# Kernel optimization log

Hardware: AMD Instinct MI355X
Metric: run time of the kernel (lower is better)

Reference implementation:

```python
import jax, jax.numpy as jnp
import numpy as np

N = 100000
F_IN = 128
HIDDEN = 64
HEADS = 4
EPS = 1e-16
SLOPE = 0.2  # PyG GATConv default negative_slope


def gat_conv(x, src, dst, W, a_src, a_dst, b, heads, out_ch, concat, n_nodes):
    # x: [N, F]; W: [F, heads*out_ch]; a_src/a_dst: [heads, out_ch]
    h = (x @ W).reshape(n_nodes, heads, out_ch)              # [N, H, C]
    alpha_s = jnp.einsum('nhc,hc->nh', h, a_src)             # [N, H]
    alpha_d = jnp.einsum('nhc,hc->nh', h, a_dst)             # [N, H]
    e = alpha_s[src] + alpha_d[dst]                          # [E, H]
    e = jnp.where(e > 0, e, SLOPE * e)                       # leaky_relu
    # segment softmax over destination node
    m = jax.ops.segment_max(e, dst, num_segments=n_nodes)    # [N, H]
    m = jnp.where(jnp.isfinite(m), m, 0.0)                   # empty segments
    ex = jnp.exp(e - m[dst])                                 # [E, H]
    denom = jax.ops.segment_sum(ex, dst, num_segments=n_nodes)  # [N, H]
    alpha = ex / (denom[dst] + EPS)                          # [E, H]
    # weighted scatter-aggregate of source features at destinations
    msg = h[src] * alpha[:, :, None]                         # [E, H, C]
    out = jax.ops.segment_sum(msg, dst, num_segments=n_nodes)  # [N, H, C]
    if concat:
        out = out.reshape(n_nodes, heads * out_ch)
    else:
        out = out.mean(axis=1)
    return out + b


def setup_inputs() -> dict:
    key = jax.random.key(0)
    ks = jax.random.split(key, 12)
    x = jax.random.normal(ks[0], (N, F_IN), dtype=jnp.float32)
    edge_index = jax.random.randint(ks[1], (2, 1600000), 0, N, dtype=jnp.int64)
    s1 = 1.0 / np.sqrt(F_IN)
    s2 = 1.0 / np.sqrt(HIDDEN)
    return {
        'x': x,
        'edge_index': edge_index,
        'W1': jax.random.normal(ks[2], (F_IN, HIDDEN), dtype=jnp.float32) * s1,
        'a_src1': jax.random.normal(ks[3], (HEADS, HIDDEN // HEADS), dtype=jnp.float32) * s2,
        'a_dst1': jax.random.normal(ks[4], (HEADS, HIDDEN // HEADS), dtype=jnp.float32) * s2,
        'b1': jnp.zeros((HIDDEN,), dtype=jnp.float32),
        'W2': jax.random.normal(ks[5], (HIDDEN, HIDDEN), dtype=jnp.float32) * s2,
        'a_src2': jax.random.normal(ks[6], (1, HIDDEN), dtype=jnp.float32) * s2,
        'a_dst2': jax.random.normal(ks[7], (1, HIDDEN), dtype=jnp.float32) * s2,
        'b2': jnp.zeros((HIDDEN,), dtype=jnp.float32),
        'Wc': jax.random.normal(ks[8], (HIDDEN, 1), dtype=jnp.float32) * s2,
        'bc': jnp.zeros((1,), dtype=jnp.float32),
    }


def reference(x, edge_index, W1, a_src1, a_dst1, b1, W2, a_src2, a_dst2, b2, Wc, bc):
    src, dst = edge_index[0], edge_index[1]
    # dropout layers are identity in eval mode
    h = gat_conv(x, src, dst, W1, a_src1, a_dst1, b1,
                 heads=HEADS, out_ch=HIDDEN // HEADS, concat=True, n_nodes=N)
    h = jax.nn.relu(h)
    h = gat_conv(h, src, dst, W2, a_src2, a_dst2, b2,
                 heads=1, out_ch=HIDDEN, concat=False, n_nodes=N)
    h = jax.nn.relu(h)
    return h @ Wc + bc  # [N, 1]
```

## Files before the change

kernel.cpp:

```cpp
#include <hip/hip_runtime.h>
#include <hip/hip_bf16.h>


typedef __hip_bfloat16 bf16;
typedef unsigned short ushort;
typedef unsigned char uchar;
typedef __attribute__((ext_vector_type(8))) short short8;
typedef __attribute__((ext_vector_type(4))) float f32x4;

#define NN 100000
#define EE 1600000
#define BKB 9
#define BKN (1 << BKB)
#define NBK ((NN + BKN - 1) >> BKB)
#define CAP 10240
#define TILE 4096
#define EPT 16
#define NT ((EE + TILE - 1) / TILE)
#define GH 391
#define GT 782
#define BN 16
#define CHE 512

__device__ __forceinline__ float relu_np(float v) { return (v < 0.f) ? 0.f : v; }
__device__ __forceinline__ float lrelu(float v) { return v > 0.f ? v : 0.2f * v; }
__device__ __forceinline__ ushort f2bf(float f) {
    __hip_bfloat16 h = __float2bfloat16(f);
    return *reinterpret_cast<ushort*>(&h);
}
__device__ __forceinline__ float bf2f(ushort u) {
    unsigned int x = ((unsigned int)u) << 16;
    return __uint_as_float(x);
}

__device__ __forceinline__ void gemm1_body(
    int gb, ushort* wB, ushort* wE,
    const float* __restrict__ x, const float* __restrict__ W1,
    const float* __restrict__ aS, const float* __restrict__ aD,
    ushort* __restrict__ h1, float* __restrict__ as1, float* __restrict__ ad1)
{
    const int tid = threadIdx.x;
    for (int i = tid; i < 128 * 64; i += 256) {
        int k = i >> 6, n = i & 63;
        wB[n * 128 + k] = f2bf(W1[i]);
    }
    for (int i = tid; i < 128 * 16; i += 256) {
        int k = i >> 4, j = i & 15;
        float v = 0.f;
        if (j < 8) {
            int h = j & 3;
            const float* av = (j < 4) ? aS : aD;
            for (int c = 0; c < 16; ++c)
                v = fmaf(W1[k * 64 + h * 16 + c], av[h * 16 + c], v);
        }
        wE[j * 128 + k] = f2bf(v);
    }
    __syncthreads();
    const int w = tid >> 6, lane = tid & 63;
    const int m = lane & 15, quad = lane >> 4;
    const int ntiles = NN >> 4;
    for (int tile = gb * 4 + w; tile < ntiles; tile += GT * 4) {
        const int row0 = tile << 4;
        f32x4 acc[4] = {f32x4{0,0,0,0}, f32x4{0,0,0,0},
                        f32x4{0,0,0,0}, f32x4{0,0,0,0}};
        f32x4 acc5 = {0, 0, 0, 0};
        const float* xp = x + (size_t)(row0 + m) * 128 + quad * 8;
        #pragma unroll
        for (int ks = 0; ks < 128; ks += 32) {
            f32x4 x0 = *(const f32x4*)(xp + ks);
            f32x4 x1 = *(const f32x4*)(xp + ks + 4);
            short8 a;
            #pragma unroll
            for (int j = 0; j < 4; ++j) a[j] = (short)f2bf(x0[j]);
            #pragma unroll
            for (int j = 0; j < 4; ++j) a[4 + j] = (short)f2bf(x1[j]);
            #pragma unroll
            for (int t = 0; t < 4; ++t) {
                short8 b = *(const short8*)&wB[(t * 16 + m) * 128 + ks + quad * 8];
                acc[t] = __builtin_amdgcn_mfma_f32_16x16x32_bf16(a, b, acc[t], 0, 0, 0);
            }
            short8 b5 = *(const short8*)&wE[m * 128 + ks + quad * 8];
            acc5 = __builtin_amdgcn_mfma_f32_16x16x32_bf16(a, b5, acc5, 0, 0, 0);
        }
        #pragma unroll
        for (int t = 0; t < 4; ++t)
            #pragma unroll
            for (int r = 0; r < 4; ++r)
                h1[(size_t)(row0 + quad * 4 + r) * 64 + t * 16 + m] = f2bf(acc[t][r]);
        #pragma unroll
        for (int r = 0; r < 4; ++r) {
            int row = row0 + quad * 4 + r;
            if (m < 4) as1[row * 4 + m] = acc5[r];
            else if (m < 8) ad1[row * 4 + (m - 4)] = acc5[r];
        }
    }
}

__global__ __launch_bounds__(256) void k_pg(
    const int* __restrict__ src, const int* __restrict__ dst,
    int* __restrict__ gcur, int* __restrict__ pairs,
    const float* __restrict__ x, const float* __restrict__ W1,
    const float* __restrict__ aS, const float* __restrict__ aD,
    ushort* __restrict__ h1, float* __restrict__ as1, float* __restrict__ ad1,
    const float* __restrict__ W2, const float* __restrict__ aS2,
    const float* __restrict__ aD2, ushort* __restrict__ wExt)
{
    __shared__ ushort wB[64 * 128];
    __shared__ ushort wE[16 * 128];
    __shared__ int lh[NBK];
    __shared__ int lbase[NBK];
    const int bid = blockIdx.x;
    const int tid = threadIdx.x;

    if (bid < NT) {
        for (int i = tid; i < NBK; i += 256) lh[i] = 0;
        __syncthreads();
        const int e0 = bid * TILE;
        int pk[EPT], bk[EPT], rv[EPT];
        #pragma unroll
        for (int j = 0; j < EPT; ++j) {
            int e = e0 + j * 256 + tid;
            if (e < EE) {
                int d = dst[e];
                bk[j] = d >> BKB;
                pk[j] = src[e] | ((d & (BKN - 1)) << 17);
                rv[j] = atomicAdd(&lh[bk[j]], 1);
            }
        }
        __syncthreads();
        for (int i = tid; i < NBK; i += 256)
            lbase[i] = lh[i] ? atomicAdd(&gcur[i], lh[i]) : 0;
        __syncthreads();
        #pragma unroll
        for (int j = 0; j < EPT; ++j) {
            int e = e0 + j * 256 + tid;
            if (e < EE)
                pairs[(size_t)bk[j] * CAP + lbase[bk[j]] + rv[j]] = pk[j];
        }
    } else if (bid < NT + GH) {
        gemm1_body(bid - NT, wB, wE, x, W1, aS, aD, h1, as1, ad1);
    } else {
        for (int i = tid; i < 80 * 64; i += 256) {
            int n = i >> 6, k = i & 63;
            float v = 0.f;
            if (n < 64) {
                v = W2[k * 64 + n];
            } else if (n == 64) {
                for (int c = 0; c < 64; ++c) v = fmaf(W2[k * 64 + c], aS2[c], v);
            } else if (n == 65) {
                for (int c = 0; c < 64; ++c) v = fmaf(W2[k * 64 + c], aD2[c], v);
            }
            wExt[i] = f2bf(v);
        }
    }
}

__global__ __launch_bounds__(256) void k_bg(
    const int* __restrict__ gcur, const int* __restrict__ pairs,
    int* __restrict__ row_ptr, uchar* __restrict__ rcnt,
    int* __restrict__ col,
    const float* __restrict__ x, const float* __restrict__ W1,
    const float* __restrict__ aS, const float* __restrict__ aD,
    ushort* __restrict__ h1, float* __restrict__ as1, float* __restrict__ ad1)
{
    __shared__ ushort wB[64 * 128];
    __shared__ ushort wE[16 * 128];
    __shared__ int hist[BKN];
    __shared__ int sP[256];
    const int bid = blockIdx.x;
    const int tid = threadIdx.x;

    if (bid >= NBK) {
        gemm1_body(bid - NBK + GH, wB, wE, x, W1, aS, aD, h1, as1, ad1);
        return;
    }

    const int b = bid;
    const int n0 = b << BKB;
    const int base = b * CAP, endE = base + gcur[b];
    for (int i = tid; i < BKN; i += 256) hist[i] = 0;
    __syncthreads();
    for (int i = base + tid; i < endE; i += 256)
        atomicAdd(&hist[pairs[i] >> 17], 1);
    __syncthreads();
    int a0 = hist[2 * tid], a1 = hist[2 * tid + 1];
    int tot = a0 + a1;
    sP[tid] = tot;
    __syncthreads();
    for (int off = 1; off < 256; off <<= 1) {
        int t = (tid >= off) ? sP[tid - off] : 0;
        __syncthreads();
        sP[tid] += t;
        __syncthreads();
    }
    const int excl = sP[tid] - tot;
    const int c0 = base + excl;
    hist[2 * tid] = c0;
    hist[2 * tid + 1] = c0 + a0;
    if (n0 + 2 * tid < NN) {
        row_ptr[n0 + 2 * tid] = c0;
        rcnt[n0 + 2 * tid] = (uchar)a0;
    }
    if (n0 + 2 * tid + 1 < NN) {
        row_ptr[n0 + 2 * tid + 1] = c0 + a0;
        rcnt[n0 + 2 * tid + 1] = (uchar)a1;
    }
    __syncthreads();
    for (int i = base + tid; i < endE; i += 256) {
        int pr = pairs[i];
        int p = atomicAdd(&hist[pr >> 17], 1);
        col[p] = pr & 0x1FFFF;
    }
}

__global__ __launch_bounds__(256, 8) void k_seg1f(
    const int* __restrict__ rp, const uchar* __restrict__ rcnt,
    const int* __restrict__ col,
    const float* __restrict__ as1, const float* __restrict__ ad1,
    const ushort* __restrict__ h1, const float* __restrict__ b1,
    const ushort* __restrict__ wExt,
    ushort* __restrict__ h2, float* __restrict__ as2, float* __restrict__ ad2,
    int N)
{
    __shared__ __align__(16) ushort zS[BN * 72];
    __shared__ float pS[CHE * 4];
    __shared__ int colS[CHE];
    __shared__ uchar ndS[CHE];
    __shared__ int sRp[BN + 1];
    __shared__ float bS[64];
    __shared__ float adS[BN * 4];

    const int tid = threadIdx.x;
    const int n0 = blockIdx.x * BN;

    if (tid < 64) bS[tid] = b1[tid];
    if (tid < BN * 4) adS[tid] = ad1[(size_t)n0 * 4 + tid];
    if (tid < BN) sRp[tid] = rp[n0 + tid];
    if (tid == BN) sRp[BN] = rp[n0 + BN - 1] + (int)rcnt[n0 + BN - 1];
    __syncthreads();

    const int eb0 = sRp[0];
    const int cnt = min(sRp[BN] - eb0, CHE);

    for (int t = tid; t < cnt; t += 256) {
        int ge = eb0 + t;
        colS[t] = col[ge];
        int nd = 0;
        #pragma unroll
        for (int k = 1; k < BN; ++k) nd += (ge >= sRp[k]);
        ndS[t] = (uchar)nd;
    }
    __syncthreads();
    for (int t = tid; t < cnt * 4; t += 256) {
        int e = t >> 2, hh = t & 3;
        float v = as1[(size_t)colS[e] * 4 + hh] + adS[ndS[e] * 4 + hh];
        pS[t] = __expf(lrelu(v));
    }
    __syncthreads();

    const int w = tid >> 6, lane = tid & 63;
    const int g = lane >> 4, c4 = lane & 15, head = c4 >> 2;
    const int nb = w * 4 + g;
    const int s_n = sRp[nb] - eb0, e_n = sRp[nb + 1] - eb0;

    f32x4 acc = {0, 0, 0, 0};
    float den = 0.f;
    int i = s_n;
    for (; i + 3 < e_n; i += 4) {
        int cA = colS[i], cB = colS[i + 1], cC = colS[i + 2], cD = colS[i + 3];
        ushort4 hA = *(const ushort4*)&h1[(size_t)cA * 64 + c4 * 4];
        ushort4 hB = *(const ushort4*)&h1[(size_t)cB * 64 + c4 * 4];
        ushort4 hC = *(const ushort4*)&h1[(size_t)cC * 64 + c4 * 4];
        ushort4 hD = *(const ushort4*)&h1[(size_t)cD * 64 + c4 * 4];
        float pA = pS[(i + 0) * 4 + head], pB = pS[(i + 1) * 4 + head];
        float pC = pS[(i + 2) * 4 + head], pD = pS[(i + 3) * 4 + head];
        den += (pA + pB) + (pC + pD);
        acc[0] = fmaf(pA, bf2f(hA.x), acc[0]);
        acc[1] = fmaf(pA, bf2f(hA.y), acc[1]);
        acc[2] = fmaf(pA, bf2f(hA.z), acc[2]);
        acc[3] = fmaf(pA, bf2f(hA.w), acc[3]);
        acc[0] = fmaf(pB, bf2f(hB.x), acc[0]);
        acc[1] = fmaf(pB, bf2f(hB.y), acc[1]);
        acc[2] = fmaf(pB, bf2f(hB.z), acc[2]);
        acc[3] = fmaf(pB, bf2f(hB.w), acc[3]);
        acc[0] = fmaf(pC, bf2f(hC.x), acc[0]);
        acc[1] = fmaf(pC, bf2f(hC.y), acc[1]);
        acc[2] = fmaf(pC, bf2f(hC.z), acc[2]);
        acc[3] = fmaf(pC, bf2f(hC.w), acc[3]);
        acc[0] = fmaf(pD, bf2f(hD.x), acc[0]);
        acc[1] = fmaf(pD, bf2f(hD.y), acc[1]);
        acc[2] = fmaf(pD, bf2f(hD.z), acc[2]);
        acc[3] = fmaf(pD, bf2f(hD.w), acc[3]);
    }
    for (; i < e_n; ++i) {
        int cA = colS[i];
        ushort4 hA = *(const ushort4*)&h1[(size_t)cA * 64 + c4 * 4];
        float pA = pS[i * 4 + head];
        den += pA;
        acc[0] = fmaf(pA, bf2f(hA.x), acc[0]);
        acc[1] = fmaf(pA, bf2f(hA.y), acc[1]);
        acc[2] = fmaf(pA, bf2f(hA.z), acc[2]);
        acc[3] = fmaf(pA, bf2f(hA.w), acc[3]);
    }
    {
        float inv = 1.f / (den + 1e-16f);
        ushort4 zv;
        zv.x = f2bf(relu_np(acc[0] * inv + bS[c4 * 4 + 0]));
        zv.y = f2bf(relu_np(acc[1] * inv + bS[c4 * 4 + 1]));
        zv.z = f2bf(relu_np(acc[2] * inv + bS[c4 * 4 + 2]));
        zv.w = f2bf(relu_np(acc[3] * inv + bS[c4 * 4 + 3]));
        *(ushort4*)&zS[nb * 72 + c4 * 4] = zv;
    }
    __syncthreads();

    const int m = c4, quad = g;
    for (int t = w; t < 5; t += 4) {
        f32x4 acct = {0, 0, 0, 0};
        #pragma unroll
        for (int ks = 0; ks < 64; ks += 32) {
            short8 a = *(const short8*)&zS[m * 72 + ks + quad * 8];
            short8 b = *(const short8*)&wExt[(t * 16 + m) * 64 + ks + quad * 8];
            acct = __builtin_amdgcn_mfma_f32_16x16x32_bf16(a, b, acct, 0, 0, 0);
        }
        if (t < 4) {
            #pragma unroll
            for (int r = 0; r < 4; ++r)
                h2[(size_t)(n0 + quad * 4 + r) * 64 + t * 16 + m] = f2bf(acct[r]);
        } else {
            #pragma unroll
            for (int r = 0; r < 4; ++r) {
                int row = n0 + quad * 4 + r;
                if (m == 0) as2[row] = acct[r];
                else if (m == 1) ad2[row] = acct[r];
            }
        }
    }
}

__global__ __launch_bounds__(256, 8) void k_seg2f(
    const int* __restrict__ rp, const uchar* __restrict__ rcnt,
    const int* __restrict__ col,
    const float* __restrict__ as2, const float* __restrict__ ad2,
    const ushort* __restrict__ h2, const float* __restrict__ b2,
    const float* __restrict__ Wc, const float* __restrict__ bc,
    float* __restrict__ out, int N)
{
    __shared__ float pS[CHE];
    __shared__ int colS[CHE];
    __shared__ uchar ndS[CHE];
    __shared__ int sRp[BN + 1];
    __shared__ float adS[BN];
    __shared__ float b2S[64];
    __shared__ float wcS[64];

    const int tid = threadIdx.x;
    const int n0 = blockIdx.x * BN;
    if (tid < 64) { b2S[tid] = b2[tid]; wcS[tid] = Wc[tid]; }
    if (tid < BN) { sRp[tid] = rp[n0 + tid]; adS[tid] = ad2[n0 + tid]; }
    if (tid == BN) sRp[BN] = rp[n0 + BN - 1] + (int)rcnt[n0 + BN - 1];
    __syncthreads();

    const int eb0 = sRp[0];
    const int cnt = min(sRp[BN] - eb0, CHE);
    for (int t = tid; t < cnt; t += 256) {
        int ge = eb0 + t;
        colS[t] = col[ge];
        int nd = 0;
        #pragma unroll
        for (int k = 1; k < BN; ++k) nd += (ge >= sRp[k]);
        ndS[t] = (uchar)nd;
    }
    __syncthreads();
    for (int t = tid; t < cnt; t += 256)
        pS[t] = __expf(lrelu(as2[colS[t]] + adS[ndS[t]]));
    __syncthreads();

    const int w = tid >> 6, lane = tid & 63;
    const int g = lane >> 4, c4 = lane & 15;
    const int nb = w * 4 + g;
    const int myn = n0 + nb;
    const int s_n = sRp[nb] - eb0, e_n = sRp[nb + 1] - eb0;

    f32x4 acc = {0, 0, 0, 0};
    float den = 0.f;
    int i = s_n;
    for (; i + 3 < e_n; i += 4) {
        int cA = colS[i], cB = colS[i + 1], cC = colS[i + 2], cD = colS[i + 3];
        ushort4 hA = *(const ushort4*)&h2[(size_t)cA * 64 + c4 * 4];
        ushort4 hB = *(const ushort4*)&h2[(size_t)cB * 64 + c4 * 4];
        ushort4 hC = *(const ushort4*)&h2[(size_t)cC * 64 + c4 * 4];
        ushort4 hD = *(const ushort4*)&h2[(size_t)cD * 64 + c4 * 4];
        float pA = pS[i + 0], pB = pS[i + 1], pC = pS[i + 2], pD = pS[i + 3];
        den += (pA + pB) + (pC + pD);
        acc[0] = fmaf(pA, bf2f(hA.x), acc[0]);
        acc[1] = fmaf(pA, bf2f(hA.y), acc[1]);
        acc[2] = fmaf(pA, bf2f(hA.z), acc[2]);
        acc[3] = fmaf(pA, bf2f(hA.w), acc[3]);
        acc[0] = fmaf(pB, bf2f(hB.x), acc[0]);
        acc[1] = fmaf(pB, bf2f(hB.y), acc[1]);
        acc[2] = fmaf(pB, bf2f(hB.z), acc[2]);
        acc[3] = fmaf(pB, bf2f(hB.w), acc[3]);
        acc[0] = fmaf(pC, bf2f(hC.x), acc[0]);
        acc[1] = fmaf(pC, bf2f(hC.y), acc[1]);
        acc[2] = fmaf(pC, bf2f(hC.z), acc[2]);
        acc[3] = fmaf(pC, bf2f(hC.w), acc[3]);
        acc[0] = fmaf(pD, bf2f(hD.x), acc[0]);
        acc[1] = fmaf(pD, bf2f(hD.y), acc[1]);
        acc[2] = fmaf(pD, bf2f(hD.z), acc[2]);
        acc[3] = fmaf(pD, bf2f(hD.w), acc[3]);
    }
    for (; i < e_n; ++i) {
        int cA = colS[i];
        ushort4 hA = *(const ushort4*)&h2[(size_t)cA * 64 + c4 * 4];
        float pA = pS[i];
        den += pA;
        acc[0] = fmaf(pA, bf2f(hA.x), acc[0]);
        acc[1] = fmaf(pA, bf2f(hA.y), acc[1]);
        acc[2] = fmaf(pA, bf2f(hA.z), acc[2]);
        acc[3] = fmaf(pA, bf2f(hA.w), acc[3]);
    }

    float inv = 1.f / (den + 1e-16f);
    float t2 = 0.f;
    #pragma unroll
    for (int j = 0; j < 4; ++j)
        t2 += relu_np(acc[j] * inv + b2S[c4 * 4 + j]) * wcS[c4 * 4 + j];
    t2 += __shfl_xor(t2, 1);
    t2 += __shfl_xor(t2, 2);
    t2 += __shfl_xor(t2, 4);
    t2 += __shfl_xor(t2, 8);
    if (c4 == 0) out[myn] = t2 + bc[0];
}

extern "C" void kernel_launch(void* const* d_in, const int* in_sizes, int n_in,
                              void* d_out, int out_size, void* d_ws, size_t ws_size,
                              hipStream_t stream)
{
    const float* x   = (const float*)d_in[0];
    const int*   ei  = (const int*)d_in[1];
    const float* W1  = (const float*)d_in[2];
    const float* aS1 = (const float*)d_in[3];
    const float* aD1 = (const float*)d_in[4];
    const float* b1  = (const float*)d_in[5];
    const float* W2  = (const float*)d_in[6];
    const float* aS2 = (const float*)d_in[7];
    const float* aD2 = (const float*)d_in[8];
    const float* b2  = (const float*)d_in[9];
    const float* Wc  = (const float*)d_in[10];
    const float* bc  = (const float*)d_in[11];
    float* out = (float*)d_out;

    const int N = NN;
    const int E = EE;
    const int* src = ei;
    const int* dst = ei + E;

    ushort* h1   = (ushort*)d_ws;
    ushort* h2   = h1 + (size_t)N * 64;
    float*  as1  = (float*)(h2 + (size_t)N * 64);
    float*  ad1  = as1 + (size_t)N * 4;
    float*  as2  = ad1 + (size_t)N * 4;
    float*  ad2  = as2 + (size_t)N;
    ushort* wExt = (ushort*)(ad2 + (size_t)N);
    int* row_ptr = (int*)(wExt + 80 * 64);
    uchar* rcnt  = (uchar*)(row_ptr + N);
    int* gcur    = (int*)(rcnt + ((N + 3) & ~3));
    int* col     = gcur + NBK;
    int* pairs   = (int*)h2;

    hipMemsetAsync(gcur, 0, NBK * sizeof(int), stream);

    k_pg<<<NT + GH + 1, 256, 0, stream>>>(src, dst, gcur, pairs,
                                          x, W1, aS1, aD1, h1, as1, ad1,
                                          W2, aS2, aD2, wExt);

    k_bg<<<NBK + GH, 256, 0, stream>>>(gcur, pairs, row_ptr, rcnt, col,
                                       x, W1, aS1, aD1, h1, as1, ad1);

    k_seg1f<<<N / BN, 256, 0, stream>>>(row_ptr, rcnt, col, as1, ad1, h1, b1,
                                        wExt, h2, as2, ad2, N);

    k_seg2f<<<N / BN, 256, 0, stream>>>(row_ptr, rcnt, col, as2, ad2, h2,
                                        b2, Wc, bc, out, N);
}
```

Baseline: 252.6 us.

## Fuse all GAT stages into one persistent cooperative kernel with grid syncs

```diff
diff --git a/kernel.cpp b/kernel.cpp
--- a/kernel.cpp
+++ b/kernel.cpp
@@ -1,5 +1,8 @@
 #include <hip/hip_runtime.h>
 #include <hip/hip_bf16.h>
+#include <hip/hip_cooperative_groups.h>
+
+namespace cg = cooperative_groups;
 
 
 typedef __hip_bfloat16 bf16;
@@ -17,10 +20,11 @@
 #define TILE 4096
 #define EPT 16
 #define NT ((EE + TILE - 1) / TILE)
-#define GH 391
 #define GT 782
 #define BN 16
 #define CHE 512
+#define NGRP (NN / BN)
+#define MGRID 1280
 
 __device__ __forceinline__ float relu_np(float v) { return (v < 0.f) ? 0.f : v; }
 __device__ __forceinline__ float lrelu(float v) { return v > 0.f ? v : 0.2f * v; }
@@ -33,8 +37,67 @@
     return __uint_as_float(x);
 }
 
+struct SmemG { ushort wB[64 * 128]; ushort wE[16 * 128]; };
+struct SmemP { int lh[NBK]; int lbase[NBK]; };
+struct SmemB { int hist[BKN]; int sP[256]; };
+struct SmemS1 {
+    ushort zS[BN * 72];
+    float pS[CHE * 4];
+    int colS[CHE];
+    int sRp[BN + 1];
+    float bS[64];
+    float adS[BN * 4];
+    uchar ndS[CHE];
+};
+struct SmemS2 {
+    float pS[CHE];
+    int colS[CHE];
+    int sRp[BN + 1];
+    float adS[BN];
+    float b2S[64];
+    float wcS[64];
+    uchar ndS[CHE];
+};
+union __align__(16) Smem { SmemG g; SmemP p; SmemB b; SmemS1 s1; SmemS2 s2; };
+
+__device__ __forceinline__ void zero_body(int* __restrict__ gcur)
+{
+    for (int i = threadIdx.x; i < NBK; i += 256) gcur[i] = 0;
+}
+
+__device__ __forceinline__ void part_body(
+    int u, SmemP& sp, const int* __restrict__ src, const int* __restrict__ dst,
+    int* __restrict__ gcur, int* __restrict__ pairs)
+{
+    const int tid = threadIdx.x;
+    for (int i = tid; i < NBK; i += 256) sp.lh[i] = 0;
+    __syncthreads();
+    const int e0 = u * TILE;
+    int pk[EPT], bk[EPT], rv[EPT];
+    #pragma unroll
+    for (int j = 0; j < EPT; ++j) {
+        int e = e0 + j * 256 + tid;
+        if (e < EE) {
+            int d = dst[e];
+            bk[j] = d >> BKB;
+            pk[j] = src[e] | ((d & (BKN - 1)) << 17);
+            rv[j] = atomicAdd(&sp.lh[bk[j]], 1);
+        }
+    }
+    __syncthreads();
+    for (int i = tid; i < NBK; i += 256)
+        sp.lbase[i] = sp.lh[i] ? atomicAdd(&gcur[i], sp.lh[i]) : 0;
+    __syncthreads();
+    #pragma unroll
+    for (int j = 0; j < EPT; ++j) {
+        int e = e0 + j * 256 + tid;
+        if (e < EE)
+            pairs[(size_t)bk[j] * CAP + sp.lbase[bk[j]] + rv[j]] = pk[j];
+    }
+}
+
 __device__ __forceinline__ void gemm1_body(
-    int gb, ushort* wB, ushort* wE,
+    int gb, SmemG& sg,
     const float* __restrict__ x, const float* __restrict__ W1,
     const float* __restrict__ aS, const float* __restrict__ aD,
     ushort* __restrict__ h1, float* __restrict__ as1, float* __restrict__ ad1)
@@ -42,7 +105,7 @@
     const int tid = threadIdx.x;
     for (int i = tid; i < 128 * 64; i += 256) {
         int k = i >> 6, n = i & 63;
-        wB[n * 128 + k] = f2bf(W1[i]);
+        sg.wB[n * 128 + k] = f2bf(W1[i]);
     }
     for (int i = tid; i < 128 * 16; i += 256) {
         int k = i >> 4, j = i & 15;
@@ -53,7 +116,7 @@
             for (int c = 0; c < 16; ++c)
                 v = fmaf(W1[k * 64 + h * 16 + c], av[h * 16 + c], v);
         }
-        wE[j * 128 + k] = f2bf(v);
+        sg.wE[j * 128 + k] = f2bf(v);
     }
     __syncthreads();
     const int w = tid >> 6, lane = tid & 63;
@@ -76,10 +139,10 @@
             for (int j = 0; j < 4; ++j) a[4 + j] = (short)f2bf(x1[j]);
             #pragma unroll
             for (int t = 0; t < 4; ++t) {
-                short8 b = *(const short8*)&wB[(t * 16 + m) * 128 + ks + quad * 8];
+                short8 b = *(const short8*)&sg.wB[(t * 16 + m) * 128 + ks + quad * 8];
                 acc[t] = __builtin_amdgcn_mfma_f32_16x16x32_bf16(a, b, acc[t], 0, 0, 0);
             }
-            short8 b5 = *(const short8*)&wE[m * 128 + ks + quad * 8];
+            short8 b5 = *(const short8*)&sg.wE[m * 128 + ks + quad * 8];
             acc5 = __builtin_amdgcn_mfma_f32_16x16x32_bf16(a, b5, acc5, 0, 0, 0);
         }
         #pragma unroll
@@ -96,107 +159,50 @@
     }
 }
 
-__global__ __launch_bounds__(256) void k_pg(
-    const int* __restrict__ src, const int* __restrict__ dst,
-    int* __restrict__ gcur, int* __restrict__ pairs,
-    const float* __restrict__ x, const float* __restrict__ W1,
-    const float* __restrict__ aS, const float* __restrict__ aD,
-    ushort* __restrict__ h1, float* __restrict__ as1, float* __restrict__ ad1,
+__device__ __forceinline__ void wext_body(
     const float* __restrict__ W2, const float* __restrict__ aS2,
     const float* __restrict__ aD2, ushort* __restrict__ wExt)
 {
-    __shared__ ushort wB[64 * 128];
-    __shared__ ushort wE[16 * 128];
-    __shared__ int lh[NBK];
-    __shared__ int lbase[NBK];
-    const int bid = blockIdx.x;
+    for (int i = threadIdx.x; i < 80 * 64; i += 256) {
+        int n = i >> 6, k = i & 63;
+        float v = 0.f;
+        if (n < 64) {
+            v = W2[k * 64 + n];
+        } else if (n == 64) {
+            for (int c = 0; c < 64; ++c) v = fmaf(W2[k * 64 + c], aS2[c], v);
+        } else if (n == 65) {
+            for (int c = 0; c < 64; ++c) v = fmaf(W2[k * 64 + c], aD2[c], v);
+        }
+        wExt[i] = f2bf(v);
+    }
+}
+
+__device__ __forceinline__ void bucket_body(
+    int b, SmemB& sb, const int* __restrict__ gcur, const int* __restrict__ pairs,
+    int* __restrict__ row_ptr, uchar* __restrict__ rcnt, int* __restrict__ col)
+{
+    const int n0 = b << BKB;
     const int tid = threadIdx.x;
-
-    if (bid < NT) {
-        for (int i = tid; i < NBK; i += 256) lh[i] = 0;
+    const int base = b * CAP, endE = base + gcur[b];
+    for (int i = tid; i < BKN; i += 256) sb.hist[i] = 0;
+    __syncthreads();
+    for (int i = base + tid; i < endE; i += 256)
+        atomicAdd(&sb.hist[pairs[i] >> 17], 1);
+    __syncthreads();
+    int a0 = sb.hist[2 * tid], a1 = sb.hist[2 * tid + 1];
+    int tot = a0 + a1;
+    sb.sP[tid] = tot;
+    __syncthreads();
+    for (int off = 1; off < 256; off <<= 1) {
+        int t = (tid >= off) ? sb.sP[tid - off] : 0;
         __syncthreads();
-        const int e0 = bid * TILE;
-        int pk[EPT], bk[EPT], rv[EPT];
-        #pragma unroll
-        for (int j = 0; j < EPT; ++j) {
-            int e = e0 + j * 256 + tid;
-            if (e < EE) {
-                int d = dst[e];
-                bk[j] = d >> BKB;
-                pk[j] = src[e] | ((d & (BKN - 1)) << 17);
-                rv[j] = atomicAdd(&lh[bk[j]], 1);
-            }
-        }
+        sb.sP[tid] += t;
         __syncthreads();
-        for (int i = tid; i < NBK; i += 256)
-            lbase[i] = lh[i] ? atomicAdd(&gcur[i], lh[i]) : 0;
-        __syncthreads();
-        #pragma unroll
-        for (int j = 0; j < EPT; ++j) {
-            int e = e0 + j * 256 + tid;
-            if (e < EE)
-                pairs[(size_t)bk[j] * CAP + lbase[bk[j]] + rv[j]] = pk[j];
-        }
-    } else if (bid < NT + GH) {
-        gemm1_body(bid - NT, wB, wE, x, W1, aS, aD, h1, as1, ad1);
-    } else {
-        for (int i = tid; i < 80 * 64; i += 256) {
-            int n = i >> 6, k = i & 63;
-            float v = 0.f;
-            if (n < 64) {
-                v = W2[k * 64 + n];
-            } else if (n == 64) {
-                for (int c = 0; c < 64; ++c) v = fmaf(W2[k * 64 + c], aS2[c], v);
-            } else if (n == 65) {
-                for (int c = 0; c < 64; ++c) v = fmaf(W2[k * 64 + c], aD2[c], v);
-            }
-            wExt[i] = f2bf(v);
-        }
-    }
-}
-
-__global__ __launch_bounds__(256) void k_bg(
-    const int* __restrict__ gcur, const int* __restrict__ pairs,
-    int* __restrict__ row_ptr, uchar* __restrict__ rcnt,
-    int* __restrict__ col,
-    const float* __restrict__ x, const float* __restrict__ W1,
-    const float* __restrict__ aS, const float* __restrict__ aD,
-    ushort* __restrict__ h1, float* __restrict__ as1, float* __restrict__ ad1)
-{
-    __shared__ ushort wB[64 * 128];
-    __shared__ ushort wE[16 * 128];
-    __shared__ int hist[BKN];
-    __shared__ int sP[256];
-    const int bid = blockIdx.x;
-    const int tid = threadIdx.x;
-
-    if (bid >= NBK) {
-        gemm1_body(bid - NBK + GH, wB, wE, x, W1, aS, aD, h1, as1, ad1);
-        return;
-    }
-
-    const int b = bid;
-    const int n0 = b << BKB;
-    const int base = b * CAP, endE = base + gcur[b];
-    for (int i = tid; i < BKN; i += 256) hist[i] = 0;
-    __syncthreads();
-    for (int i = base + tid; i < endE; i += 256)
-        atomicAdd(&hist[pairs[i] >> 17], 1);
-    __syncthreads();
-    int a0 = hist[2 * tid], a1 = hist[2 * tid + 1];
-    int tot = a0 + a1;
-    sP[tid] = tot;
-    __syncthreads();
-    for (int off = 1; off < 256; off <<= 1) {
-        int t = (tid >= off) ? sP[tid - off] : 0;
-        __syncthreads();
-        sP[tid] += t;
-        __syncthreads();
-    }
-    const int excl = sP[tid] - tot;
+    }
+    const int excl = sb.sP[tid] - tot;
     const int c0 = base + excl;
-    hist[2 * tid] = c0;
-    hist[2 * tid + 1] = c0 + a0;
+    sb.hist[2 * tid] = c0;
+    sb.hist[2 * tid + 1] = c0 + a0;
     if (n0 + 2 * tid < NN) {
         row_ptr[n0 + 2 * tid] = c0;
         rcnt[n0 + 2 * tid] = (uchar)a0;
@@ -208,72 +214,61 @@
     __syncthreads();
     for (int i = base + tid; i < endE; i += 256) {
         int pr = pairs[i];
-        int p = atomicAdd(&hist[pr >> 17], 1);
+        int p = atomicAdd(&sb.hist[pr >> 17], 1);
         col[p] = pr & 0x1FFFF;
     }
 }
 
-__global__ __launch_bounds__(256, 8) void k_seg1f(
-    const int* __restrict__ rp, const uchar* __restrict__ rcnt,
-    const int* __restrict__ col,
-    const float* __restrict__ as1, const float* __restrict__ ad1,
-    const ushort* __restrict__ h1, const float* __restrict__ b1,
-    const ushort* __restrict__ wExt,
-    ushort* __restrict__ h2, float* __restrict__ as2, float* __restrict__ ad2,
-    int N)
-{
-    __shared__ __align__(16) ushort zS[BN * 72];
-    __shared__ float pS[CHE * 4];
-    __shared__ int colS[CHE];
-    __shared__ uchar ndS[CHE];
-    __shared__ int sRp[BN + 1];
-    __shared__ float bS[64];
-    __shared__ float adS[BN * 4];
-
+__device__ __forceinline__ void seg1_body(
+    int grp, SmemS1& s, const int* __restrict__ rp, const uchar* __restrict__ rcnt,
+    const int* __restrict__ col, const float* __restrict__ as1,
+    const float* __restrict__ ad1, const ushort* __restrict__ h1,
+    const ushort* __restrict__ wExt, ushort* __restrict__ h2,
+    float* __restrict__ as2, float* __restrict__ ad2)
+{
     const int tid = threadIdx.x;
-    const int n0 = blockIdx.x * BN;
-
-    if (tid < 64) bS[tid] = b1[tid];
-    if (tid < BN * 4) adS[tid] = ad1[(size_t)n0 * 4 + tid];
-    if (tid < BN) sRp[tid] = rp[n0 + tid];
-    if (tid == BN) sRp[BN] = rp[n0 + BN - 1] + (int)rcnt[n0 + BN - 1];
-    __syncthreads();
-
-    const int eb0 = sRp[0];
-    const int cnt = min(sRp[BN] - eb0, CHE);
+    const int n0 = grp * BN;
+
+    if (tid < BN * 4) s.adS[tid] = ad1[(size_t)n0 * 4 + tid];
+    if (tid < BN) s.sRp[tid] = rp[n0 + tid];
+    if (tid == BN) s.sRp[BN] = rp[n0 + BN - 1] + (int)rcnt[n0 + BN - 1];
+    __syncthreads();
+
+    const int eb0 = s.sRp[0];
+    const int cnt = min(s.sRp[BN] - eb0, CHE);
 
     for (int t = tid; t < cnt; t += 256) {
         int ge = eb0 + t;
-        colS[t] = col[ge];
+        s.colS[t] = col[ge];
         int nd = 0;
         #pragma unroll
-        for (int k = 1; k < BN; ++k) nd += (ge >= sRp[k]);
-        ndS[t] = (uchar)nd;
+        for (int k = 1; k < BN; ++k) nd += (ge >= s.sRp[k]);
+        s.ndS[t] = (uchar)nd;
     }
     __syncthreads();
     for (int t = tid; t < cnt * 4; t += 256) {
         int e = t >> 2, hh = t & 3;
-        float v = as1[(size_t)colS[e] * 4 + hh] + adS[ndS[e] * 4 + hh];
-        pS[t] = __expf(lrelu(v));
+        float v = as1[(size_t)s.colS[e] * 4 + hh] + s.adS[s.ndS[e] * 4 + hh];
+        s.pS[t] = __expf(lrelu(v));
     }
     __syncthreads();
 
     const int w = tid >> 6, lane = tid & 63;
     const int g = lane >> 4, c4 = lane & 15, head = c4 >> 2;
     const int nb = w * 4 + g;
-    const int s_n = sRp[nb] - eb0, e_n = sRp[nb + 1] - eb0;
+    const int s_n = s.sRp[nb] - eb0, e_n = s.sRp[nb + 1] - eb0;
 
     f32x4 acc = {0, 0, 0, 0};
     float den = 0.f;
     int i = s_n;
     for (; i + 3 < e_n; i += 4) {
-        int cA = colS[i], cB = colS[i + 1], cC = colS[i + 2], cD = colS[i + 3];
+        int cA = s.colS[i], cB = s.colS[i + 1], cC = s.colS[i + 2], cD = s.colS[i + 3];
         ushort4 hA = *(const ushort4*)&h1[(size_t)cA * 64 + c4 * 4];
         ushort4 hB = *(const ushort4*)&h1[(size_t)cB * 64 + c4 * 4];
         ushort4 hC = *(const ushort4*)&h1[(size_t)cC * 64 + c4 * 4];
         ushort4 hD = *(const ushort4*)&h1[(size_t)cD * 64 + c4 * 4];
-        float pA = pS[(i + 0) * 4 + head], pB = pS[(i + 1) * 4 + head];
-        float pC = pS[(i + 2) * 4 + head], pD = pS[(i + 3) * 4 + head];
+        float pA = s.pS[(i + 0) * 4 + head], pB = s.pS[(i + 1) * 4 + head];
+        float pC = s.pS[(i + 2) * 4 + head], pD = s.pS[(i + 3) * 4 + head];
         den += (pA + pB) + (pC + pD);
         acc[0] = fmaf(pA, bf2f(hA.x), acc[0]);
         acc[1] = fmaf(pA, bf2f(hA.y), acc[1]);
@@ -293,9 +288,9 @@
         acc[3] = fmaf(pD, bf2f(hD.w), acc[3]);
     }
     for (; i < e_n; ++i) {
-        int cA = colS[i];
+        int cA = s.colS[i];
         ushort4 hA = *(const ushort4*)&h1[(size_t)cA * 64 + c4 * 4];
-        float pA = pS[i * 4 + head];
+        float pA = s.pS[i * 4 + head];
         den += pA;
         acc[0] = fmaf(pA, bf2f(hA.x), acc[0]);
         acc[1] = fmaf(pA, bf2f(hA.y), acc[1]);
@@ -305,11 +300,11 @@
     {
         float inv = 1.f / (den + 1e-16f);
         ushort4 zv;
-        zv.x = f2bf(relu_np(acc[0] * inv + bS[c4 * 4 + 0]));
-        zv.y = f2bf(relu_np(acc[1] * inv + bS[c4 * 4 + 1]));
-        zv.z = f2bf(relu_np(acc[2] * inv + bS[c4 * 4 + 2]));
-        zv.w = f2bf(relu_np(acc[3] * inv + bS[c4 * 4 + 3]));
-        *(ushort4*)&zS[nb * 72 + c4 * 4] = zv;
+        zv.x = f2bf(relu_np(acc[0] * inv + s.bS[c4 * 4 + 0]));
+        zv.y = f2bf(relu_np(acc[1] * inv + s.bS[c4 * 4 + 1]));
+        zv.z = f2bf(relu_np(acc[2] * inv + s.bS[c4 * 4 + 2]));
+        zv.w = f2bf(relu_np(acc[3] * inv + s.bS[c4 * 4 + 3]));
+        *(ushort4*)&s.zS[nb * 72 + c4 * 4] = zv;
     }
     __syncthreads();
 
@@ -318,7 +313,7 @@
         f32x4 acct = {0, 0, 0, 0};
         #pragma unroll
         for (int ks = 0; ks < 64; ks += 32) {
-            short8 a = *(const short8*)&zS[m * 72 + ks + quad * 8];
+            short8 a = *(const short8*)&s.zS[m * 72 + ks + quad * 8];
             short8 b = *(const short8*)&wExt[(t * 16 + m) * 64 + ks + quad * 8];
             acct = __builtin_amdgcn_mfma_f32_16x16x32_bf16(a, b, acct, 0, 0, 0);
         }
@@ -337,60 +332,49 @@
     }
 }
 
-__global__ __launch_bounds__(256, 8) void k_seg2f(
-    const int* __restrict__ rp, const uchar* __restrict__ rcnt,
-    const int* __restrict__ col,
-    const float* __restrict__ as2, const float* __restrict__ ad2,
-    const ushort* __restrict__ h2, const float* __restrict__ b2,
-    const float* __restrict__ Wc, const float* __restrict__ bc,
-    float* __restrict__ out, int N)
-{
-    __shared__ float pS[CHE];
-    __shared__ int colS[CHE];
-    __shared__ uchar ndS[CHE];
-    __shared__ int sRp[BN + 1];
-    __shared__ float adS[BN];
-    __shared__ float b2S[64];
-    __shared__ float wcS[64];
-
+__device__ __forceinline__ void seg2_body(
+    int grp, SmemS2& s, const int* __restrict__ rp, const uchar* __restrict__ rcnt,
+    const int* __restrict__ col, const float* __restrict__ as2,
+    const float* __restrict__ ad2, const ushort* __restrict__ h2,
+    const float* __restrict__ bc, float* __restrict__ out)
+{
     const int tid = threadIdx.x;
-    const int n0 = blockIdx.x * BN;
-    if (tid < 64) { b2S[tid] = b2[tid]; wcS[tid] = Wc[tid]; }
-    if (tid < BN) { sRp[tid] = rp[n0 + tid]; adS[tid] = ad2[n0 + tid]; }
-    if (tid == BN) sRp[BN] = rp[n0 + BN - 1] + (int)rcnt[n0 + BN - 1];
-    __syncthreads();
-
-    const int eb0 = sRp[0];
-    const int cnt = min(sRp[BN] - eb0, CHE);
+    const int n0 = grp * BN;
+    if (tid < BN) { s.sRp[tid] = rp[n0 + tid]; s.adS[tid] = ad2[n0 + tid]; }
+    if (tid == BN) s.sRp[BN] = rp[n0 + BN - 1] + (int)rcnt[n0 + BN - 1];
+    __syncthreads();
+
+    const int eb0 = s.sRp[0];
+    const int cnt = min(s.sRp[BN] - eb0, CHE);
     for (int t = tid; t < cnt; t += 256) {
         int ge = eb0 + t;
-        colS[t] = col[ge];
+        s.colS[t] = col[ge];
         int nd = 0;
         #pragma unroll
-        for (int k = 1; k < BN; ++k) nd += (ge >= sRp[k]);
-        ndS[t] = (uchar)nd;
+        for (int k = 1; k < BN; ++k) nd += (ge >= s.sRp[k]);
+        s.ndS[t] = (uchar)nd;
     }
     __syncthreads();
     for (int t = tid; t < cnt; t += 256)
-        pS[t] = __expf(lrelu(as2[colS[t]] + adS[ndS[t]]));
+        s.pS[t] = __expf(lrelu(as2[s.colS[t]] + s.adS[s.ndS[t]]));
     __syncthreads();
 
     const int w = tid >> 6, lane = tid & 63;
     const int g = lane >> 4, c4 = lane & 15;
     const int nb = w * 4 + g;
     const int myn = n0 + nb;
-    const int s_n = sRp[nb] - eb0, e_n = sRp[nb + 1] - eb0;
+    const int s_n = s.sRp[nb] - eb0, e_n = s.sRp[nb + 1] - eb0;
 
     f32x4 acc = {0, 0, 0, 0};
     float den = 0.f;
     int i = s_n;
     for (; i + 3 < e_n; i += 4) {
-        int cA = colS[i], cB = colS[i + 1], cC = colS[i + 2], cD = colS[i + 3];
+        int cA = s.colS[i], cB = s.colS[i + 1], cC = s.colS[i + 2], cD = s.colS[i + 3];
         ushort4 hA = *(const ushort4*)&h2[(size_t)cA * 64 + c4 * 4];
         ushort4 hB = *(const ushort4*)&h2[(size_t)cB * 64 + c4 * 4];
         ushort4 hC = *(const ushort4*)&h2[(size_t)cC * 64 + c4 * 4];
         ushort4 hD = *(const ushort4*)&h2[(size_t)cD * 64 + c4 * 4];
-        float pA = pS[i + 0], pB = pS[i + 1], pC = pS[i + 2], pD = pS[i + 3];
+        float pA = s.pS[i + 0], pB = s.pS[i + 1], pC = s.pS[i + 2], pD = s.pS[i + 3];
         den += (pA + pB) + (pC + pD);
         acc[0] = fmaf(pA, bf2f(hA.x), acc[0]);
         acc[1] = fmaf(pA, bf2f(hA.y), acc[1]);
@@ -410,9 +394,9 @@
         acc[3] = fmaf(pD, bf2f(hD.w), acc[3]);
     }
     for (; i < e_n; ++i) {
-        int cA = colS[i];
+        int cA = s.colS[i];
         ushort4 hA = *(const ushort4*)&h2[(size_t)cA * 64 + c4 * 4];
-        float pA = pS[i];
+        float pA = s.pS[i];
         den += pA;
         acc[0] = fmaf(pA, bf2f(hA.x), acc[0]);
         acc[1] = fmaf(pA, bf2f(hA.y), acc[1]);
@@ -424,12 +408,66 @@
     float t2 = 0.f;
     #pragma unroll
     for (int j = 0; j < 4; ++j)
-        t2 += relu_np(acc[j] * inv + b2S[c4 * 4 + j]) * wcS[c4 * 4 + j];
+        t2 += relu_np(acc[j] * inv + s.b2S[c4 * 4 + j]) * s.wcS[c4 * 4 + j];
     t2 += __shfl_xor(t2, 1);
     t2 += __shfl_xor(t2, 2);
     t2 += __shfl_xor(t2, 4);
     t2 += __shfl_xor(t2, 8);
     if (c4 == 0) out[myn] = t2 + bc[0];
+}
+
+__global__ __launch_bounds__(256, 5) void k_fused(
+    int phase,
+    const int* __restrict__ src, const int* __restrict__ dst,
+    int* __restrict__ gcur, int* __restrict__ pairs,
+    const float* __restrict__ x, const float* __restrict__ W1,
+    const float* __restrict__ aS1, const float* __restrict__ aD1,
+    ushort* __restrict__ h1, float* __restrict__ as1, float* __restrict__ ad1,
+    const float* __restrict__ W2, const float* __restrict__ aS2,
+    const float* __restrict__ aD2, ushort* __restrict__ wExt,
+    int* __restrict__ row_ptr, uchar* __restrict__ rcnt, int* __restrict__ col,
+    const float* __restrict__ b1, ushort* __restrict__ h2,
+    float* __restrict__ as2, float* __restrict__ ad2,
+    const float* __restrict__ b2, const float* __restrict__ Wc,
+    const float* __restrict__ bc, float* __restrict__ out)
+{
+    __shared__ Smem sm;
+    const bool mono = (phase < 0);
+    const int bid = blockIdx.x;
+    const int tid = threadIdx.x;
+
+    if (mono || phase == 0) {
+        if (bid == 0) zero_body(gcur);
+    }
+    if (mono) cg::this_grid().sync();
+
+    if (mono || phase == 1) {
+        for (int u = bid; u < NT + GT + 1; u += gridDim.x) {
+            if (u < NT) part_body(u, sm.p, src, dst, gcur, pairs);
+            else if (u < NT + GT) gemm1_body(u - NT, sm.g, x, W1, aS1, aD1, h1, as1, ad1);
+            else wext_body(W2, aS2, aD2, wExt);
+        }
+    }
+    if (mono) cg::this_grid().sync();
+
+    if (mono || phase == 2) {
+        for (int b = bid; b < NBK; b += gridDim.x)
+            bucket_body(b, sm.b, gcur, pairs, row_ptr, rcnt, col);
+    }
+    if (mono) cg::this_grid().sync();
+
+    if (mono || phase == 3) {
+        if (tid < 64) sm.s1.bS[tid] = b1[tid];
+        for (int g = bid; g < NGRP; g += gridDim.x)
+            seg1_body(g, sm.s1, row_ptr, rcnt, col, as1, ad1, h1, wExt, h2, as2, ad2);
+    }
+    if (mono) cg::this_grid().sync();
+
+    if (mono || phase == 4) {
+        if (tid < 64) { sm.s2.b2S[tid] = b2[tid]; sm.s2.wcS[tid] = Wc[tid]; }
+        for (int g = bid; g < NGRP; g += gridDim.x)
+            seg2_body(g, sm.s2, row_ptr, rcnt, col, as2, ad2, h2, bc, out);
+    }
 }
 
 extern "C" void kernel_launch(void* const* d_in, const int* in_sizes, int n_in,
@@ -450,36 +488,51 @@
     const float* bc  = (const float*)d_in[11];
     float* out = (float*)d_out;
 
-    const int N = NN;
-    const int E = EE;
     const int* src = ei;
-    const int* dst = ei + E;
+    const int* dst = ei + EE;
 
     ushort* h1   = (ushort*)d_ws;
-    ushort* h2   = h1 + (size_t)N * 64;
-    float*  as1  = (float*)(h2 + (size_t)N * 64);
-    float*  ad1  = as1 + (size_t)N * 4;
-    float*  as2  = ad1 + (size_t)N * 4;
-    float*  ad2  = as2 + (size_t)N;
-    ushort* wExt = (ushort*)(ad2 + (size_t)N);
+    ushort* h2   = h1 + (size_t)NN * 64;
+    float*  as1  = (float*)(h2 + (size_t)NN * 64);
+    float*  ad1  = as1 + (size_t)NN * 4;
+    float*  as2  = ad1 + (size_t)NN * 4;
+    float*  ad2  = as2 + (size_t)NN;
+    ushort* wExt = (ushort*)(ad2 + (size_t)NN);
     int* row_ptr = (int*)(wExt + 80 * 64);
-    uchar* rcnt  = (uchar*)(row_ptr + N);
-    int* gcur    = (int*)(rcnt + ((N + 3) & ~3));
+    uchar* rcnt  = (uchar*)(row_ptr + NN);
+    int* gcur    = (int*)(rcnt + ((NN + 3) & ~3));
     int* col     = gcur + NBK;
     int* pairs   = (int*)h2;
 
-    hipMemsetAsync(gcur, 0, NBK * sizeof(int), stream);
-
-    k_pg<<<NT + GH + 1, 256, 0, stream>>>(src, dst, gcur, pairs,
-                                          x, W1, aS1, aD1, h1, as1, ad1,
-                                          W2, aS2, aD2, wExt);
-
-    k_bg<<<NBK + GH, 256, 0, stream>>>(gcur, pairs, row_ptr, rcnt, col,
-                                       x, W1, aS1, aD1, h1, as1, ad1);
-
-    k_seg1f<<<N / BN, 256, 0, stream>>>(row_ptr, rcnt, col, as1, ad1, h1, b1,
-                                        wExt, h2, as2, ad2, N);
-
-    k_seg2f<<<N / BN, 256, 0, stream>>>(row_ptr, rcnt, col, as2, ad2, h2,
-                                        b2, Wc, bc, out, N);
-}
+    int ph = -1;
+    void* args[] = {&ph, &src, &dst, &gcur, &pairs, &x, &W1, &aS1, &aD1,
+                    &h1, &as1, &ad1, &W2, &aS2, &aD2, &wExt,
+                    &row_ptr, &rcnt, &col, &b1, &h2, &as2, &ad2,
+                    &b2, &Wc, &bc, &out};
+    hipError_t err = hipLaunchCooperativeKernel(
+        (const void*)k_fused, dim3(MGRID), dim3(256), args, 0, stream);
+
+    if (err != hipSuccess) {
+        (void)hipGetLastError();
+        k_fused<<<1, 256, 0, stream>>>(0, src, dst, gcur, pairs, x, W1, aS1, aD1,
+                                       h1, as1, ad1, W2, aS2, aD2, wExt,
+                                       row_ptr, rcnt, col, b1, h2, as2, ad2,
+                                       b2, Wc, bc, out);
+        k_fused<<<NT + GT + 1, 256, 0, stream>>>(1, src, dst, gcur, pairs, x, W1,
+                                       aS1, aD1, h1, as1, ad1, W2, aS2, aD2, wExt,
+                                       row_ptr, rcnt, col, b1, h2, as2, ad2,
+                                       b2, Wc, bc, out);
+        k_fused<<<NBK, 256, 0, stream>>>(2, src, dst, gcur, pairs, x, W1, aS1, aD1,
+                                       h1, as1, ad1, W2, aS2, aD2, wExt,
+                                       row_ptr, rcnt, col, b1, h2, as2, ad2,
+                                       b2, Wc, bc, out);
+        k_fused<<<NGRP, 256, 0, stream>>>(3, src, dst, gcur, pairs, x, W1, aS1, aD1,
+                                       h1, as1, ad1, W2, aS2, aD2, wExt,
+                                       row_ptr, rcnt, col, b1, h2, as2, ad2,
+                                       b2, Wc, bc, out);
+        k_fused<<<NGRP, 256, 0, stream>>>(4, src, dst, gcur, pairs, x, W1, aS1, aD1,
+                                       h1, as1, ad1, W2, aS2, aD2, wExt,
+                                       row_ptr, rcnt, col, b1, h2, as2, ad2,
+                                       b2, Wc, bc, out);
+    }
+}
```

New measurement: 847.6 us. 3.36x slower.

## Merge partition and bucket-sort kernels into one launch with device-wide completion flag

Applied to the files above, without the earlier changes.

```diff
diff --git a/kernel.cpp b/kernel.cpp
--- a/kernel.cpp
+++ b/kernel.cpp
@@ -17,10 +17,11 @@
 #define TILE 4096
 #define EPT 16
 #define NT ((EE + TILE - 1) / TILE)
-#define GH 391
 #define GT 782
 #define BN 16
 #define CHE 512
+#define NGRP (NN / BN)
+#define PGB_GRID (NT + GT + 1 + NBK)
 
 __device__ __forceinline__ float relu_np(float v) { return (v < 0.f) ? 0.f : v; }
 __device__ __forceinline__ float lrelu(float v) { return v > 0.f ? v : 0.2f * v; }
@@ -32,9 +33,48 @@
     unsigned int x = ((unsigned int)u) << 16;
     return __uint_as_float(x);
 }
+__device__ __forceinline__ int load_acq(const int* p) {
+    return __hip_atomic_load(p, __ATOMIC_ACQUIRE, __HIP_MEMORY_SCOPE_AGENT);
+}
+
+struct SmemG { ushort wB[64 * 128]; ushort wE[16 * 128]; };
+struct SmemP { int lh[NBK]; int lbase[NBK]; };
+struct SmemB { int hist[BKN]; int sP[256]; };
+union __align__(16) SmemF { SmemG g; SmemP p; SmemB b; };
+
+__device__ __forceinline__ void part_body(
+    int u, SmemP& sp, const int* __restrict__ src, const int* __restrict__ dst,
+    int* __restrict__ gcur, int* __restrict__ pairs)
+{
+    const int tid = threadIdx.x;
+    for (int i = tid; i < NBK; i += 256) sp.lh[i] = 0;
+    __syncthreads();
+    const int e0 = u * TILE;
+    int pk[EPT], bk[EPT], rv[EPT];
+    #pragma unroll
+    for (int j = 0; j < EPT; ++j) {
+        int e = e0 + j * 256 + tid;
+        if (e < EE) {
+            int d = dst[e];
+            bk[j] = d >> BKB;
+            pk[j] = src[e] | ((d & (BKN - 1)) << 17);
+            rv[j] = atomicAdd(&sp.lh[bk[j]], 1);
+        }
+    }
+    __syncthreads();
+    for (int i = tid; i < NBK; i += 256)
+        sp.lbase[i] = sp.lh[i] ? atomicAdd(&gcur[i], sp.lh[i]) : 0;
+    __syncthreads();
+    #pragma unroll
+    for (int j = 0; j < EPT; ++j) {
+        int e = e0 + j * 256 + tid;
+        if (e < EE)
+            pairs[(size_t)bk[j] * CAP + sp.lbase[bk[j]] + rv[j]] = pk[j];
+    }
+}
 
 __device__ __forceinline__ void gemm1_body(
-    int gb, ushort* wB, ushort* wE,
+    int gb, SmemG& sg,
     const float* __restrict__ x, const float* __restrict__ W1,
     const float* __restrict__ aS, const float* __restrict__ aD,
     ushort* __restrict__ h1, float* __restrict__ as1, float* __restrict__ ad1)
@@ -42,7 +82,7 @@
     const int tid = threadIdx.x;
     for (int i = tid; i < 128 * 64; i += 256) {
         int k = i >> 6, n = i & 63;
-        wB[n * 128 + k] = f2bf(W1[i]);
+        sg.wB[n * 128 + k] = f2bf(W1[i]);
     }
     for (int i = tid; i < 128 * 16; i += 256) {
         int k = i >> 4, j = i & 15;
@@ -53,7 +93,7 @@
             for (int c = 0; c < 16; ++c)
                 v = fmaf(W1[k * 64 + h * 16 + c], av[h * 16 + c], v);
         }
-        wE[j * 128 + k] = f2bf(v);
+        sg.wE[j * 128 + k] = f2bf(v);
     }
     __syncthreads();
     const int w = tid >> 6, lane = tid & 63;
@@ -76,10 +116,10 @@
             for (int j = 0; j < 4; ++j) a[4 + j] = (short)f2bf(x1[j]);
             #pragma unroll
             for (int t = 0; t < 4; ++t) {
-                short8 b = *(const short8*)&wB[(t * 16 + m) * 128 + ks + quad * 8];
+                short8 b = *(const short8*)&sg.wB[(t * 16 + m) * 128 + ks + quad * 8];
                 acc[t] = __builtin_amdgcn_mfma_f32_16x16x32_bf16(a, b, acc[t], 0, 0, 0);
             }
-            short8 b5 = *(const short8*)&wE[m * 128 + ks + quad * 8];
+            short8 b5 = *(const short8*)&sg.wE[m * 128 + ks + quad * 8];
             acc5 = __builtin_amdgcn_mfma_f32_16x16x32_bf16(a, b5, acc5, 0, 0, 0);
         }
         #pragma unroll
@@ -96,50 +136,73 @@
     }
 }
 
-__global__ __launch_bounds__(256) void k_pg(
+__device__ __forceinline__ void bucket_body(
+    int b, SmemB& sb, const int* __restrict__ gcur, const int* __restrict__ pairs,
+    int* __restrict__ row_ptr, uchar* __restrict__ rcnt, int* __restrict__ col)
+{
+    const int n0 = b << BKB;
+    const int tid = threadIdx.x;
+    const int base = b * CAP, endE = base + load_acq(&gcur[b]);
+    for (int i = tid; i < BKN; i += 256) sb.hist[i] = 0;
+    __syncthreads();
+    for (int i = base + tid; i < endE; i += 256)
+        atomicAdd(&sb.hist[pairs[i] >> 17], 1);
+    __syncthreads();
+    int a0 = sb.hist[2 * tid], a1 = sb.hist[2 * tid + 1];
+    int tot = a0 + a1;
+    sb.sP[tid] = tot;
+    __syncthreads();
+    for (int off = 1; off < 256; off <<= 1) {
+        int t = (tid >= off) ? sb.sP[tid - off] : 0;
+        __syncthreads();
+        sb.sP[tid] += t;
+        __syncthreads();
+    }
+    const int excl = sb.sP[tid] - tot;
+    const int c0 = base + excl;
+    sb.hist[2 * tid] = c0;
+    sb.hist[2 * tid + 1] = c0 + a0;
+    if (n0 + 2 * tid < NN) {
+        row_ptr[n0 + 2 * tid] = c0;
+        rcnt[n0 + 2 * tid] = (uchar)a0;
+    }
+    if (n0 + 2 * tid + 1 < NN) {
+        row_ptr[n0 + 2 * tid + 1] = c0 + a0;
+        rcnt[n0 + 2 * tid + 1] = (uchar)a1;
+    }
+    __syncthreads();
+    for (int i = base + tid; i < endE; i += 256) {
+        int pr = pairs[i];
+        int p = atomicAdd(&sb.hist[pr >> 17], 1);
+        col[p] = pr & 0x1FFFF;
+    }
+}
+
+__global__ __launch_bounds__(256) void k_pgb(
     const int* __restrict__ src, const int* __restrict__ dst,
-    int* __restrict__ gcur, int* __restrict__ pairs,
+    int* __restrict__ gcur, int* __restrict__ done, int* __restrict__ pairs,
     const float* __restrict__ x, const float* __restrict__ W1,
-    const float* __restrict__ aS, const float* __restrict__ aD,
+    const float* __restrict__ aS1, const float* __restrict__ aD1,
     ushort* __restrict__ h1, float* __restrict__ as1, float* __restrict__ ad1,
     const float* __restrict__ W2, const float* __restrict__ aS2,
-    const float* __restrict__ aD2, ushort* __restrict__ wExt)
-{
-    __shared__ ushort wB[64 * 128];
-    __shared__ ushort wE[16 * 128];
-    __shared__ int lh[NBK];
-    __shared__ int lbase[NBK];
+    const float* __restrict__ aD2, ushort* __restrict__ wExt,
+    int* __restrict__ row_ptr, uchar* __restrict__ rcnt, int* __restrict__ col)
+{
+    __shared__ SmemF sm;
     const int bid = blockIdx.x;
     const int tid = threadIdx.x;
 
     if (bid < NT) {
-        for (int i = tid; i < NBK; i += 256) lh[i] = 0;
+        part_body(bid, sm.p, src, dst, gcur, pairs);
         __syncthreads();
-        const int e0 = bid * TILE;
-        int pk[EPT], bk[EPT], rv[EPT];
-        #pragma unroll
-        for (int j = 0; j < EPT; ++j) {
-            int e = e0 + j * 256 + tid;
-            if (e < EE) {
-                int d = dst[e];
-                bk[j] = d >> BKB;
-                pk[j] = src[e] | ((d & (BKN - 1)) << 17);
-                rv[j] = atomicAdd(&lh[bk[j]], 1);
-            }
-        }
-        __syncthreads();
-        for (int i = tid; i < NBK; i += 256)
-            lbase[i] = lh[i] ? atomicAdd(&gcur[i], lh[i]) : 0;
-        __syncthreads();
-        #pragma unroll
-        for (int j = 0; j < EPT; ++j) {
-            int e = e0 + j * 256 + tid;
-            if (e < EE)
-                pairs[(size_t)bk[j] * CAP + lbase[bk[j]] + rv[j]] = pk[j];
-        }
-    } else if (bid < NT + GH) {
-        gemm1_body(bid - NT, wB, wE, x, W1, aS, aD, h1, as1, ad1);
-    } else {
+        if (tid == 0) {
+            __threadfence();
+            __hip_atomic_fetch_add(done, 1, __ATOMIC_RELEASE,
+                                   __HIP_MEMORY_SCOPE_AGENT);
+        }
+    } else if (bid < NT + GT) {
+        gemm1_body(bid - NT, sm.g, x, W1, aS1, aD1, h1, as1, ad1);
+    } else if (bid == NT + GT) {
         for (int i = tid; i < 80 * 64; i += 256) {
             int n = i >> 6, k = i & 63;
             float v = 0.f;
@@ -152,64 +215,13 @@
             }
             wExt[i] = f2bf(v);
         }
-    }
-}
-
-__global__ __launch_bounds__(256) void k_bg(
-    const int* __restrict__ gcur, const int* __restrict__ pairs,
-    int* __restrict__ row_ptr, uchar* __restrict__ rcnt,
-    int* __restrict__ col,
-    const float* __restrict__ x, const float* __restrict__ W1,
-    const float* __restrict__ aS, const float* __restrict__ aD,
-    ushort* __restrict__ h1, float* __restrict__ as1, float* __restrict__ ad1)
-{
-    __shared__ ushort wB[64 * 128];
-    __shared__ ushort wE[16 * 128];
-    __shared__ int hist[BKN];
-    __shared__ int sP[256];
-    const int bid = blockIdx.x;
-    const int tid = threadIdx.x;
-
-    if (bid >= NBK) {
-        gemm1_body(bid - NBK + GH, wB, wE, x, W1, aS, aD, h1, as1, ad1);
-        return;
-    }
-
-    const int b = bid;
-    const int n0 = b << BKB;
-    const int base = b * CAP, endE = base + gcur[b];
-    for (int i = tid; i < BKN; i += 256) hist[i] = 0;
-    __syncthreads();
-    for (int i = base + tid; i < endE; i += 256)
-        atomicAdd(&hist[pairs[i] >> 17], 1);
-    __syncthreads();
-    int a0 = hist[2 * tid], a1 = hist[2 * tid + 1];
-    int tot = a0 + a1;
-    sP[tid] = tot;
-    __syncthreads();
-    for (int off = 1; off < 256; off <<= 1) {
-        int t = (tid >= off) ? sP[tid - off] : 0;
+    } else {
+        if (tid == 0) {
+            while (load_acq(done) < NT) __builtin_amdgcn_s_sleep(16);
+        }
         __syncthreads();
-        sP[tid] += t;
-        __syncthreads();
-    }
-    const int excl = sP[tid] - tot;
-    const int c0 = base + excl;
-    hist[2 * tid] = c0;
-    hist[2 * tid + 1] = c0 + a0;
-    if (n0 + 2 * tid < NN) {
-        row_ptr[n0 + 2 * tid] = c0;
-        rcnt[n0 + 2 * tid] = (uchar)a0;
-    }
-    if (n0 + 2 * tid + 1 < NN) {
-        row_ptr[n0 + 2 * tid + 1] = c0 + a0;
-        rcnt[n0 + 2 * tid + 1] = (uchar)a1;
-    }
-    __syncthreads();
-    for (int i = base + tid; i < endE; i += 256) {
-        int pr = pairs[i];
-        int p = atomicAdd(&hist[pr >> 17], 1);
-        col[p] = pr & 0x1FFFF;
+        __threadfence();
+        bucket_body(bid - (NT + GT + 1), sm.b, gcur, pairs, row_ptr, rcnt, col);
     }
 }
 
@@ -219,8 +231,7 @@
     const float* __restrict__ as1, const float* __restrict__ ad1,
     const ushort* __restrict__ h1, const float* __restrict__ b1,
     const ushort* __restrict__ wExt,
-    ushort* __restrict__ h2, float* __restrict__ as2, float* __restrict__ ad2,
-    int N)
+    ushort* __restrict__ h2, float* __restrict__ as2, float* __restrict__ ad2)
 {
     __shared__ __align__(16) ushort zS[BN * 72];
     __shared__ float pS[CHE * 4];
@@ -343,7 +354,7 @@
     const float* __restrict__ as2, const float* __restrict__ ad2,
     const ushort* __restrict__ h2, const float* __restrict__ b2,
     const float* __restrict__ Wc, const float* __restrict__ bc,
-    float* __restrict__ out, int N)
+    float* __restrict__ out)
 {
     __shared__ float pS[CHE];
     __shared__ int colS[CHE];
@@ -450,36 +461,33 @@
     const float* bc  = (const float*)d_in[11];
     float* out = (float*)d_out;
 
-    const int N = NN;
-    const int E = EE;
     const int* src = ei;
-    const int* dst = ei + E;
+    const int* dst = ei + EE;
 
     ushort* h1   = (ushort*)d_ws;
-    ushort* h2   = h1 + (size_t)N * 64;
-    float*  as1  = (float*)(h2 + (size_t)N * 64);
-    float*  ad1  = as1 + (size_t)N * 4;
-    float*  as2  = ad1 + (size_t)N * 4;
-    float*  ad2  = as2 + (size_t)N;
-    ushort* wExt = (ushort*)(ad2 + (size_t)N);
+    ushort* h2   = h1 + (size_t)NN * 64;
+    float*  as1  = (float*)(h2 + (size_t)NN * 64);
+    float*  ad1  = as1 + (size_t)NN * 4;
+    float*  as2  = ad1 + (size_t)NN * 4;
+    float*  ad2  = as2 + (size_t)NN;
+    ushort* wExt = (ushort*)(ad2 + (size_t)NN);
     int* row_ptr = (int*)(wExt + 80 * 64);
-    uchar* rcnt  = (uchar*)(row_ptr + N);
-    int* gcur    = (int*)(rcnt + ((N + 3) & ~3));
-    int* col     = gcur + NBK;
+    uchar* rcnt  = (uchar*)(row_ptr + NN);
+    int* gcur    = (int*)(rcnt + ((NN + 3) & ~3));
+    int* done    = gcur + NBK;
+    int* col     = done + 1;
     int* pairs   = (int*)h2;
 
-    hipMemsetAsync(gcur, 0, NBK * sizeof(int), stream);
-
-    k_pg<<<NT + GH + 1, 256, 0, stream>>>(src, dst, gcur, pairs,
-                                          x, W1, aS1, aD1, h1, as1, ad1,
-                                          W2, aS2, aD2, wExt);
-
-    k_bg<<<NBK + GH, 256, 0, stream>>>(gcur, pairs, row_ptr, rcnt, col,
-                                       x, W1, aS1, aD1, h1, as1, ad1);
-
-    k_seg1f<<<N / BN, 256, 0, stream>>>(row_ptr, rcnt, col, as1, ad1, h1, b1,
-                                        wExt, h2, as2, ad2, N);
-
-    k_seg2f<<<N / BN, 256, 0, stream>>>(row_ptr, rcnt, col, as2, ad2, h2,
-                                        b2, Wc, bc, out, N);
-}
+    hipMemsetAsync(gcur, 0, (NBK + 1) * sizeof(int), stream);
+
+    k_pgb<<<PGB_GRID, 256, 0, stream>>>(src, dst, gcur, done, pairs,
+                                        x, W1, aS1, aD1, h1, as1, ad1,
+                                        W2, aS2, aD2, wExt,
+                                        row_ptr, rcnt, col);
+
+    k_seg1f<<<NGRP, 256, 0, stream>>>(row_ptr, rcnt, col, as1, ad1, h1, b1,
+                                      wExt, h2, as2, ad2);
+
+    k_seg2f<<<NGRP, 256, 0, stream>>>(row_ptr, rcnt, col, as2, ad2, h2,
+                                      b2, Wc, bc, out);
+}
```

Result: slower. 313.5 us (+24.1%).
